# Optimization experiments

Measured on AMD Instinct MI355X. Metric: run time of the kernel, lower is better.

Reference implementation:

```python
import jax, jax.numpy as jnp
import numpy as np

EMBED = 512
HEADS = 8
HEAD_D = EMBED // HEADS
N = 16
QLEN = 512
KLEN = 512


def _relative_keys(Wr, q_len, k_len):
    # Transformer-XL style sinusoid table of size (q_len + k_len)
    max_dist = q_len + k_len
    inv_freqs = 10000.0 ** (-jnp.arange(0, EMBED, 2, dtype=jnp.float32) / EMBED)
    seq = jnp.arange(max_dist, dtype=jnp.float32)[:, None] * inv_freqs[None, :]
    pos_emb = jnp.concatenate([jnp.sin(seq), jnp.cos(seq)], axis=-1)  # [max_dist, E]
    rel = (pos_emb @ Wr.T).reshape(max_dist, HEADS, HEAD_D)           # [max_dist, H, D]
    # query_offset defaults to key_len
    q_pos = jnp.arange(q_len)[:, None] + k_len
    k_pos = jnp.arange(k_len)[None, :]
    rel_idx = jnp.clip(q_pos - k_pos, 0, max_dist - 1)                # [q, k]
    return rel[rel_idx]                                               # [q, k, H, D]


def setup_inputs() -> dict:
    key = jax.random.key(0)
    ks = jax.random.split(key, 12)
    s = 0.02
    return {
        "values": jax.random.normal(ks[0], (N, KLEN, EMBED), jnp.float32),
        "keys": jax.random.normal(ks[1], (N, KLEN, EMBED), jnp.float32),
        "query": jax.random.normal(ks[2], (N, QLEN, EMBED), jnp.float32),
        "mask": jnp.ones((N, QLEN, KLEN), jnp.int32),
        "Wv": jax.random.normal(ks[3], (HEAD_D, HEAD_D), jnp.float32) * s,
        "Wk": jax.random.normal(ks[4], (HEAD_D, HEAD_D), jnp.float32) * s,
        "Wq": jax.random.normal(ks[5], (HEAD_D, HEAD_D), jnp.float32) * s,
        "Wr": jax.random.normal(ks[6], (EMBED, EMBED), jnp.float32) * s,
        "u_bias": jax.random.normal(ks[7], (HEADS, HEAD_D), jnp.float32) * s,
        "v_bias": jax.random.normal(ks[8], (HEADS, HEAD_D), jnp.float32) * s,
        "Wo": jax.random.normal(ks[9], (EMBED, EMBED), jnp.float32) * s,
        "bo": jnp.zeros((EMBED,), jnp.float32),
    }


def reference(values, keys, query, mask, Wv, Wk, Wq, Wr, u_bias, v_bias, Wo, bo):
    # per-head projections (same D x D weight shared across heads, torch Linear: x @ W.T)
    v = values.reshape(N, KLEN, HEADS, HEAD_D) @ Wv.T
    k = keys.reshape(N, KLEN, HEADS, HEAD_D) @ Wk.T
    q = query.reshape(N, QLEN, HEADS, HEAD_D) @ Wq.T

    rel_keys = _relative_keys(Wr, QLEN, KLEN)  # [q, k, H, D]

    content = jnp.einsum("nqhd,nkhd->nhqk", q + u_bias, k)
    position = jnp.einsum("nqhd,qkhd->nhqk", q + v_bias, rel_keys)
    energy = content + position
    energy = jnp.where(mask[:, None, :, :] == 0, jnp.float32(-1e20), energy)

    attn = jax.nn.softmax(energy / (float(HEAD_D) ** 0.5), axis=3)  # [N,H,q,k]
    out = jnp.einsum("nhqk,nkhd->nqhd", attn, v).reshape(N, QLEN, EMBED)
    out = out @ Wo.T + bo
    return out, attn
```

## Files before the change

### kernel.cpp

```cpp
#include <hip/hip_runtime.h>
#include <math.h>

#define NB     16
#define HEADS  8
#define HD     64
#define EMBED  512
#define QL     512
#define KL     512

#define WS_QU   0
#define WS_QV   2097152
#define WS_KB   4194304
#define WS_VT   6291456
#define WS_PEB  8388608
#define WS_RELB 8912896
#define WS_OH   9175040

typedef __attribute__((ext_vector_type(8))) short bf16x8;
typedef __attribute__((ext_vector_type(4))) float f32x4;
typedef __attribute__((ext_vector_type(8))) unsigned short ushort8v;
typedef __attribute__((ext_vector_type(4))) unsigned short ushort4v;

#define MFMA16 __builtin_amdgcn_mfma_f32_16x16x32_bf16

static __device__ __forceinline__ unsigned short f2bf(float x) {
    unsigned u = __builtin_bit_cast(unsigned, x);
    u += 0x7fffu + ((u >> 16) & 1u);
    return (unsigned short)(u >> 16);
}

static __device__ __forceinline__ bf16x8 pack8(f32x4 a, f32x4 b) {
    union { bf16x8 v; unsigned u[4]; } r;
    asm("v_cvt_pk_bf16_f32 %0, %1, %2" : "=v"(r.u[0]) : "v"(a[0]), "v"(a[1]));
    asm("v_cvt_pk_bf16_f32 %0, %1, %2" : "=v"(r.u[1]) : "v"(a[2]), "v"(a[3]));
    asm("v_cvt_pk_bf16_f32 %0, %1, %2" : "=v"(r.u[2]) : "v"(b[0]), "v"(b[1]));
    asm("v_cvt_pk_bf16_f32 %0, %1, %2" : "=v"(r.u[3]) : "v"(b[2]), "v"(b[3]));
    return r.v;
}

__global__ void pe_kernel(unsigned short* __restrict__ peb) {
    int j = blockIdx.x;
    int i = threadIdx.x;
    float invf = exp2f(-(float)i * (13.287712379549449f / 256.0f));
    float ang  = (float)j * invf;
    peb[j * 512 + i]       = f2bf(sinf(ang));
    peb[j * 512 + 256 + i] = f2bf(cosf(ang));
}

__global__ __launch_bounds__(256) void rel_kernel(const unsigned short* __restrict__ peb,
                                                  const float* __restrict__ Wr,
                                                  unsigned short* __restrict__ relb) {
    __shared__ __align__(16) unsigned short At[64][64];
    __shared__ __align__(16) unsigned short Bt[64][64];
    int bm = blockIdx.x >> 3, bn = blockIdx.x & 7;
    int tid = threadIdx.x;
    int w = tid >> 6, lane = tid & 63;
    int fr = lane & 15, fg = lane >> 4;
    f32x4 acc[4] = {};
    for (int kk = 0; kk < 512; kk += 64) {
        __syncthreads();
        for (int p = 0; p < 2; ++p) {
            int idx = tid + 256 * p;
            int row = idx >> 3, slot = idx & 7;
            *(bf16x8*)&At[row][((slot ^ (row & 7))) * 8] =
                *(const bf16x8*)&peb[(bm * 64 + row) * 512 + kk + slot * 8];
        }
        for (int p = 0; p < 4; ++p) {
            int idx = tid + 256 * p;
            int row = idx >> 4, c4 = idx & 15;
            float4 v = *(const float4*)&Wr[(bn * 64 + row) * 512 + kk + c4 * 4];
            ushort4v pk;
            pk[0] = f2bf(v.x); pk[1] = f2bf(v.y); pk[2] = f2bf(v.z); pk[3] = f2bf(v.w);
            int slot = c4 >> 1, rem = (c4 & 1) * 4;
            *(ushort4v*)&Bt[row][((slot ^ (row & 7))) * 8 + rem] = pk;
        }
        __syncthreads();
        bf16x8 af[2];
        int ar = w * 16 + fr;
#pragma unroll
        for (int s = 0; s < 2; ++s)
            af[s] = *(const bf16x8*)&At[ar][((fg + 4 * s) ^ (ar & 7)) * 8];
#pragma unroll
        for (int c = 0; c < 4; ++c) {
            int br = c * 16 + fr;
#pragma unroll
            for (int s = 0; s < 2; ++s) {
                bf16x8 bf = *(const bf16x8*)&Bt[br][((fg + 4 * s) ^ (br & 7)) * 8];
                acc[c] = MFMA16(af[s], bf, acc[c], 0, 0, 0);
            }
        }
    }
#pragma unroll
    for (int c = 0; c < 4; ++c)
#pragma unroll
        for (int i = 0; i < 4; ++i)
            relb[(bn * 1024 + bm * 64 + w * 16 + fg * 4 + i) * 64 + c * 16 + fr] =
                f2bf(acc[c][i]);
}

__global__ __launch_bounds__(256) void proj_kernel(const float* __restrict__ query,
                                                   const float* __restrict__ keys,
                                                   const float* __restrict__ values,
                                                   const float* __restrict__ Wq,
                                                   const float* __restrict__ Wk,
                                                   const float* __restrict__ Wv,
                                                   const float* __restrict__ u_bias,
                                                   const float* __restrict__ v_bias,
                                                   float* __restrict__ ws) {
    __shared__ __align__(16) unsigned short inb[32][512];
    __shared__ __align__(16) unsigned short Wb[3][64][64];
    __shared__ __align__(16) unsigned short vtile[4][64][36];
    int n = blockIdx.x >> 4, t0 = (blockIdx.x & 15) * 32;
    int tid = threadIdx.x;
    int w = tid >> 6, lane = tid & 63;
    int fr = lane & 15, fg = lane >> 4;

    for (int p = 0; p < 3; ++p) {
        const float* Wp = (p == 0) ? Wq : (p == 1) ? Wk : Wv;
        for (int it = 0; it < 4; ++it) {
            int idx = tid + 256 * it;
            int row = idx >> 4, c4 = idx & 15;
            float4 v = *(const float4*)&Wp[row * 64 + c4 * 4];
            ushort4v pk;
            pk[0] = f2bf(v.x); pk[1] = f2bf(v.y); pk[2] = f2bf(v.z); pk[3] = f2bf(v.w);
            int slot = c4 >> 1, rem = (c4 & 1) * 4;
            *(ushort4v*)&Wb[p][row][((slot ^ (row & 7))) * 8 + rem] = pk;
        }
    }
    unsigned short* qu_b = (unsigned short*)(ws + WS_QU);
    unsigned short* qv_b = (unsigned short*)(ws + WS_QV);
    unsigned short* k_b  = (unsigned short*)(ws + WS_KB);
    unsigned short* vT_b = (unsigned short*)(ws + WS_VT);

    for (int p = 0; p < 3; ++p) {
        const float* src = (p == 0) ? query : (p == 1) ? keys : values;
        __syncthreads();
        for (int it = 0; it < 16; ++it) {
            int idx = tid + 256 * it;
            int row = idx >> 7, c4 = idx & 127;
            float4 v = *(const float4*)&src[((long)(n * 512 + t0 + row)) * 512 + c4 * 4];
            ushort4v pk;
            pk[0] = f2bf(v.x); pk[1] = f2bf(v.y); pk[2] = f2bf(v.z); pk[3] = f2bf(v.w);
            int slot = c4 >> 1, rem = (c4 & 1) * 4;
            *(ushort4v*)&inb[row][((slot ^ (row & 7))) * 8 + rem] = pk;
        }
        __syncthreads();
        for (int hh = 0; hh < 2; ++hh) {
            int h = w * 2 + hh, nh = n * 8 + h;
            bf16x8 af[2][2];
#pragma unroll
            for (int tt = 0; tt < 2; ++tt) {
                int ar = tt * 16 + fr;
#pragma unroll
                for (int s = 0; s < 2; ++s)
                    af[tt][s] = *(const bf16x8*)&inb[ar][(h * 8 + ((fg + 4 * s) ^ (ar & 7))) * 8];
            }
            f32x4 acc[2][4] = {};
#pragma unroll
            for (int dt = 0; dt < 4; ++dt) {
                int br = dt * 16 + fr;
                bf16x8 bf[2];
#pragma unroll
                for (int s = 0; s < 2; ++s)
                    bf[s] = *(const bf16x8*)&Wb[p][br][((fg + 4 * s) ^ (br & 7)) * 8];
#pragma unroll
                for (int tt = 0; tt < 2; ++tt)
#pragma unroll
                    for (int s = 0; s < 2; ++s)
                        acc[tt][dt] = MFMA16(af[tt][s], bf[s], acc[tt][dt], 0, 0, 0);
            }
            if (p == 0) {
#pragma unroll
                for (int dt = 0; dt < 4; ++dt) {
                    float ub = u_bias[h * 64 + dt * 16 + fr];
                    float vb = v_bias[h * 64 + dt * 16 + fr];
#pragma unroll
                    for (int tt = 0; tt < 2; ++tt)
#pragma unroll
                        for (int i = 0; i < 4; ++i) {
                            long o = ((long)(nh * 512 + t0 + tt * 16 + fg * 4 + i)) * 64 +
                                     dt * 16 + fr;
                            qu_b[o] = f2bf(acc[tt][dt][i] + ub);
                            qv_b[o] = f2bf(acc[tt][dt][i] + vb);
                        }
                }
            } else if (p == 1) {
#pragma unroll
                for (int dt = 0; dt < 4; ++dt)
#pragma unroll
                    for (int tt = 0; tt < 2; ++tt)
#pragma unroll
                        for (int i = 0; i < 4; ++i)
                            k_b[((long)(nh * 512 + t0 + tt * 16 + fg * 4 + i)) * 64 +
                                dt * 16 + fr] = f2bf(acc[tt][dt][i]);
            } else {
#pragma unroll
                for (int dt = 0; dt < 4; ++dt)
#pragma unroll
                    for (int tt = 0; tt < 2; ++tt)
#pragma unroll
                        for (int i = 0; i < 4; ++i)
                            vtile[w][dt * 16 + fr][tt * 16 + fg * 4 + i] =
                                f2bf(acc[tt][dt][i]);
                __syncthreads();
#pragma unroll
                for (int dg = 0; dg < 8; ++dg) {
                    int d = dg * 8 + (lane >> 3), tq = lane & 7;
                    *(ushort4v*)&vT_b[((long)(nh * 64 + d)) * 512 + t0 + tq * 4] =
                        *(const ushort4v*)&vtile[w][d][tq * 4];
                }
                __syncthreads();
            }
        }
    }
}

__global__ __launch_bounds__(512) void attn_kernel(float* __restrict__ ws,
                                                   const int* __restrict__ mask,
                                                   float* __restrict__ d_out) {
    __shared__ __align__(16) float S[32][516];
    __shared__ __align__(16) float red[4][32][17];

    const unsigned short* qu_b = (const unsigned short*)(ws + WS_QU);
    const unsigned short* qv_b = (const unsigned short*)(ws + WS_QV);
    const unsigned short* k_b  = (const unsigned short*)(ws + WS_KB);
    const unsigned short* vT_b = (const unsigned short*)(ws + WS_VT);
    const unsigned short* relb = (const unsigned short*)(ws + WS_RELB);
    unsigned short* ohb = (unsigned short*)(ws + WS_OH);
    float* attn = d_out + 4194304;

    int bid = blockIdx.x;
    int swz = (bid & 7) * 64 + (bid >> 3);
    int nh = swz >> 2, qb = swz & 3;
    int n  = nh >> 3, h = nh & 7;

    int tid  = threadIdx.x;
    int w    = tid >> 6, lane = tid & 63;
    int fr   = lane & 15, fg = lane >> 4;

    const unsigned short* kbase = k_b + (long)nh * 512 * 64;
    bf16x8 kreg[4][2];
#pragma unroll
    for (int t = 0; t < 4; ++t) {
        const unsigned short* kp = kbase + (long)(w * 64 + t * 16 + fr) * 64;
        kreg[t][0] = *(const bf16x8*)&kp[fg * 8];
        kreg[t][1] = *(const bf16x8*)&kp[(fg + 4) * 8];
    }
    int dt = w & 3, kh = w >> 2;
    const unsigned short* vp0 = vT_b + ((long)(nh * 64 + dt * 16 + fr)) * 512 + kh * 256;
    bf16x8 vreg[8];
#pragma unroll
    for (int kk = 0; kk < 8; ++kk)
        vreg[kk] = *(const bf16x8*)&vp0[kk * 32 + fg * 8];

    const unsigned short* rbase = relb + (long)h * 1024 * 64;

    for (int ti = 0; ti < 4; ++ti) {
        int q0 = qb * 128 + ti * 32;

#pragma unroll
        for (int qt = 0; qt < 2; ++qt) {
            long qa = ((long)(nh * 512 + q0 + qt * 16 + fr)) * 64;
            bf16x8 a0 = *(const bf16x8*)&qu_b[qa + fg * 8];
            bf16x8 a1 = *(const bf16x8*)&qu_b[qa + (fg + 4) * 8];
#pragma unroll
            for (int t = 0; t < 4; ++t) {
                f32x4 acc = {0.f, 0.f, 0.f, 0.f};
                acc = MFMA16(a0, kreg[t][0], acc, 0, 0, 0);
                acc = MFMA16(a1, kreg[t][1], acc, 0, 0, 0);
                int kcol = w * 64 + t * 16 + fr;
#pragma unroll
                for (int i = 0; i < 4; ++i)
                    S[qt * 16 + fg * 4 + i][kcol] = acc[i];
            }
        }
        __syncthreads();

        {
            bf16x8 qvf[2][2];
#pragma unroll
            for (int qt = 0; qt < 2; ++qt) {
                long qa = ((long)(nh * 512 + q0 + qt * 16 + fr)) * 64;
                qvf[qt][0] = *(const bf16x8*)&qv_b[qa + fg * 8];
                qvf[qt][1] = *(const bf16x8*)&qv_b[qa + (fg + 4) * 8];
            }
            for (int jt = w; jt < 34; jt += 8) {
                int jj = jt * 16 + fr;
                int j = q0 + 1 + jj;
                const unsigned short* rp = rbase + (long)j * 64;
                bf16x8 b0 = *(const bf16x8*)&rp[fg * 8];
                bf16x8 b1 = *(const bf16x8*)&rp[(fg + 4) * 8];
#pragma unroll
                for (int qt = 0; qt < 2; ++qt) {
                    f32x4 acc = {0.f, 0.f, 0.f, 0.f};
                    acc = MFMA16(qvf[qt][0], b0, acc, 0, 0, 0);
                    acc = MFMA16(qvf[qt][1], b1, acc, 0, 0, 0);
#pragma unroll
                    for (int i = 0; i < 4; ++i) {
                        int r = qt * 16 + fg * 4 + i;
                        int k = r + 511 - jj;
                        if ((unsigned)k < 512u) S[r][k] += acc[i];
                    }
                }
            }
        }
        __syncthreads();

        for (int rr = 0; rr < 4; ++rr) {
            int r = w * 4 + rr;
            const int* mrow = mask + ((long)(n * 512 + q0 + r)) * 512;
            float lg[8];
            float mx = -3.0e38f;
#pragma unroll
            for (int j = 0; j < 8; ++j) {
                int k = lane + 64 * j;
                float s = S[r][k];
                int m = mrow[k];
                float l = (m == 0) ? -1.25e19f : s * 0.125f;
                lg[j] = l;
                mx = fmaxf(mx, l);
            }
            for (int o = 32; o > 0; o >>= 1) mx = fmaxf(mx, __shfl_xor(mx, o, 64));
            float sum = 0.f;
#pragma unroll
            for (int j = 0; j < 8; ++j) { lg[j] = __expf(lg[j] - mx); sum += lg[j]; }
            for (int o = 32; o > 0; o >>= 1) sum += __shfl_xor(sum, o, 64);
            float inv = 1.0f / sum;
            float* arow = attn + ((long)(nh * 512 + q0 + r)) * 512;
#pragma unroll
            for (int j = 0; j < 8; ++j) {
                int k = lane + 64 * j;
                float p = lg[j] * inv;
                S[r][k] = p;
                arow[k] = p;
            }
        }
        __syncthreads();

        {
            f32x4 oacc[2] = {{0.f,0.f,0.f,0.f},{0.f,0.f,0.f,0.f}};
#pragma unroll
            for (int kk = 0; kk < 8; ++kk) {
#pragma unroll
                for (int qt = 0; qt < 2; ++qt) {
                    const float* sp = &S[qt * 16 + fr][kh * 256 + kk * 32 + fg * 8];
                    f32x4 a = *(const f32x4*)sp;
                    f32x4 b = *(const f32x4*)(sp + 4);
                    bf16x8 pk = pack8(a, b);
                    oacc[qt] = MFMA16(pk, vreg[kk], oacc[qt], 0, 0, 0);
                }
            }
            if (kh == 1) {
#pragma unroll
                for (int qt = 0; qt < 2; ++qt)
#pragma unroll
                    for (int i = 0; i < 4; ++i)
                        red[dt][qt * 16 + fg * 4 + i][fr] = oacc[qt][i];
            }
            __syncthreads();
            if (kh == 0) {
#pragma unroll
                for (int qt = 0; qt < 2; ++qt)
#pragma unroll
                    for (int i = 0; i < 4; ++i) {
                        float o = oacc[qt][i] + red[dt][qt * 16 + fg * 4 + i][fr];
                        ohb[((long)(n * 512 + q0 + qt * 16 + fg * 4 + i)) * 512 +
                            h * 64 + dt * 16 + fr] = f2bf(o);
                    }
            }
        }
        __syncthreads();
    }
}

__global__ __launch_bounds__(256) void wo_kernel(const float* __restrict__ ws,
                                                 const float* __restrict__ Wo,
                                                 const float* __restrict__ bo,
                                                 float* __restrict__ d_out) {
    __shared__ __align__(16) unsigned short At[128][64];
    __shared__ __align__(16) unsigned short Bt[64][64];
    const unsigned short* ohb = (const unsigned short*)(ws + WS_OH);
    int bm = blockIdx.x >> 3, bn = blockIdx.x & 7;
    int tid = threadIdx.x;
    int w = tid >> 6, lane = tid & 63;
    int fr = lane & 15, fg = lane >> 4;
    f32x4 acc[2][4] = {};
    for (int kk = 0; kk < 512; kk += 64) {
        __syncthreads();
        for (int p = 0; p < 4; ++p) {
            int idx = tid + 256 * p;
            int row = idx >> 3, slot = idx & 7;
            *(bf16x8*)&At[row][((slot ^ (row & 7))) * 8] =
                *(const bf16x8*)&ohb[(long)(bm * 128 + row) * 512 + kk + slot * 8];
        }
        for (int p = 0; p < 2; ++p) {
            int idx = tid + 256 * p;
            int row = idx >> 3, slot = idx & 7;
            const float* g = &Wo[(bn * 64 + row) * 512 + kk + slot * 8];
            float4 a = *(const float4*)g;
            float4 b = *(const float4*)(g + 4);
            ushort8v pk;
            pk[0] = f2bf(a.x); pk[1] = f2bf(a.y); pk[2] = f2bf(a.z); pk[3] = f2bf(a.w);
            pk[4] = f2bf(b.x); pk[5] = f2bf(b.y); pk[6] = f2bf(b.z); pk[7] = f2bf(b.w);
            *(ushort8v*)&Bt[row][((slot ^ (row & 7))) * 8] = pk;
        }
        __syncthreads();
        bf16x8 af[2][2], bfr[4][2];
#pragma unroll
        for (int t = 0; t < 2; ++t) {
            int ar = w * 32 + t * 16 + fr;
#pragma unroll
            for (int s = 0; s < 2; ++s)
                af[t][s] = *(const bf16x8*)&At[ar][((fg + s * 4) ^ (ar & 7)) * 8];
        }
#pragma unroll
        for (int c = 0; c < 4; ++c) {
            int br = c * 16 + fr;
#pragma unroll
            for (int s = 0; s < 2; ++s)
                bfr[c][s] = *(const bf16x8*)&Bt[br][((fg + s * 4) ^ (br & 7)) * 8];
        }
#pragma unroll
        for (int t = 0; t < 2; ++t)
#pragma unroll
            for (int c = 0; c < 4; ++c)
#pragma unroll
                for (int s = 0; s < 2; ++s)
                    acc[t][c] = MFMA16(af[t][s], bfr[c][s], acc[t][c], 0, 0, 0);
    }
#pragma unroll
    for (int t = 0; t < 2; ++t)
#pragma unroll
        for (int c = 0; c < 4; ++c) {
            int col = bn * 64 + c * 16 + fr;
            float b = bo[col];
#pragma unroll
            for (int i = 0; i < 4; ++i) {
                int row = bm * 128 + w * 32 + t * 16 + fg * 4 + i;
                d_out[(long)row * 512 + col] = acc[t][c][i] + b;
            }
        }
}

extern "C" void kernel_launch(void* const* d_in, const int* in_sizes, int n_in,
                              void* d_out, int out_size, void* d_ws, size_t ws_size,
                              hipStream_t stream) {
    const float* values = (const float*)d_in[0];
    const float* keys   = (const float*)d_in[1];
    const float* query  = (const float*)d_in[2];
    const int*   mask   = (const int*)d_in[3];
    const float* Wv     = (const float*)d_in[4];
    const float* Wk     = (const float*)d_in[5];
    const float* Wq     = (const float*)d_in[6];
    const float* Wr     = (const float*)d_in[7];
    const float* u_bias = (const float*)d_in[8];
    const float* v_bias = (const float*)d_in[9];
    const float* Wo     = (const float*)d_in[10];
    const float* bo     = (const float*)d_in[11];
    float* out = (float*)d_out;
    float* ws  = (float*)d_ws;

    unsigned short* peb  = (unsigned short*)(ws + WS_PEB);
    unsigned short* relb = (unsigned short*)(ws + WS_RELB);

    hipLaunchKernelGGL(pe_kernel,   dim3(1024),  dim3(256), 0, stream, peb);
    hipLaunchKernelGGL(rel_kernel,  dim3(128),   dim3(256), 0, stream, peb, Wr, relb);
    hipLaunchKernelGGL(proj_kernel, dim3(256),   dim3(256), 0, stream,
                       query, keys, values, Wq, Wk, Wv, u_bias, v_bias, ws);
    hipLaunchKernelGGL(attn_kernel, dim3(512),   dim3(512), 0, stream, ws, mask, out);
    hipLaunchKernelGGL(wo_kernel,   dim3(512),   dim3(256), 0, stream, ws, Wo, bo, out);
}
```

Before: 146.4 us.

## Store attention scores as swizzled bf16 in LDS and double the attention grid

The attention kernel now keeps its score tile in LDS as bf16 instead of fp32, with an XOR swizzle on columns. The grid is split into 1024 blocks of 64 queries, and K fragments are reloaded per tile instead of being held in registers. Launch bounds ask for more resident waves, and the mask, attention-row and P-fragment accesses become vectorized 8-wide operations. The aim is less LDS per block and fewer registers, so more blocks run at once and memory latency is hidden better. In exchange, content and position scores are accumulated and rounded in bf16 before the softmax, which lowers numerical precision.

```diff
diff --git a/kernel.cpp b/kernel.cpp
--- a/kernel.cpp
+++ b/kernel.cpp
@@ -27,6 +27,11 @@
     unsigned u = __builtin_bit_cast(unsigned, x);
     u += 0x7fffu + ((u >> 16) & 1u);
     return (unsigned short)(u >> 16);
+}
+
+static __device__ __forceinline__ float bf2f(unsigned short v) {
+    unsigned u = ((unsigned)v) << 16;
+    return __builtin_bit_cast(float, u);
 }
 
 static __device__ __forceinline__ bf16x8 pack8(f32x4 a, f32x4 b) {
@@ -215,10 +220,10 @@
     }
 }
 
-__global__ __launch_bounds__(512) void attn_kernel(float* __restrict__ ws,
-                                                   const int* __restrict__ mask,
-                                                   float* __restrict__ d_out) {
-    __shared__ __align__(16) float S[32][516];
+__global__ __launch_bounds__(512, 6) void attn_kernel(float* __restrict__ ws,
+                                                      const int* __restrict__ mask,
+                                                      float* __restrict__ d_out) {
+    __shared__ __align__(16) unsigned short S16[32][528];
     __shared__ __align__(16) float red[4][32][17];
 
     const unsigned short* qu_b = (const unsigned short*)(ws + WS_QU);
@@ -230,22 +235,14 @@
     float* attn = d_out + 4194304;
 
     int bid = blockIdx.x;
-    int swz = (bid & 7) * 64 + (bid >> 3);
-    int nh = swz >> 2, qb = swz & 3;
+    int swz = (bid & 7) * 128 + (bid >> 3);
+    int nh = swz >> 3, qg = swz & 7;
     int n  = nh >> 3, h = nh & 7;
 
     int tid  = threadIdx.x;
     int w    = tid >> 6, lane = tid & 63;
     int fr   = lane & 15, fg = lane >> 4;
 
-    const unsigned short* kbase = k_b + (long)nh * 512 * 64;
-    bf16x8 kreg[4][2];
-#pragma unroll
-    for (int t = 0; t < 4; ++t) {
-        const unsigned short* kp = kbase + (long)(w * 64 + t * 16 + fr) * 64;
-        kreg[t][0] = *(const bf16x8*)&kp[fg * 8];
-        kreg[t][1] = *(const bf16x8*)&kp[(fg + 4) * 8];
-    }
     int dt = w & 3, kh = w >> 2;
     const unsigned short* vp0 = vT_b + ((long)(nh * 64 + dt * 16 + fr)) * 512 + kh * 256;
     bf16x8 vreg[8];
@@ -253,25 +250,37 @@
     for (int kk = 0; kk < 8; ++kk)
         vreg[kk] = *(const bf16x8*)&vp0[kk * 32 + fg * 8];
 
+    const unsigned short* kbase = k_b + (long)nh * 512 * 64;
     const unsigned short* rbase = relb + (long)h * 1024 * 64;
 
-    for (int ti = 0; ti < 4; ++ti) {
-        int q0 = qb * 128 + ti * 32;
-
-#pragma unroll
-        for (int qt = 0; qt < 2; ++qt) {
-            long qa = ((long)(nh * 512 + q0 + qt * 16 + fr)) * 64;
-            bf16x8 a0 = *(const bf16x8*)&qu_b[qa + fg * 8];
-            bf16x8 a1 = *(const bf16x8*)&qu_b[qa + (fg + 4) * 8];
+    for (int ti = 0; ti < 2; ++ti) {
+        int q0 = qg * 64 + ti * 32;
+
+        {
+            bf16x8 qf[2][2];
+#pragma unroll
+            for (int qt = 0; qt < 2; ++qt) {
+                long qa = ((long)(nh * 512 + q0 + qt * 16 + fr)) * 64;
+                qf[qt][0] = *(const bf16x8*)&qu_b[qa + fg * 8];
+                qf[qt][1] = *(const bf16x8*)&qu_b[qa + (fg + 4) * 8];
+            }
 #pragma unroll
             for (int t = 0; t < 4; ++t) {
-                f32x4 acc = {0.f, 0.f, 0.f, 0.f};
-                acc = MFMA16(a0, kreg[t][0], acc, 0, 0, 0);
-                acc = MFMA16(a1, kreg[t][1], acc, 0, 0, 0);
                 int kcol = w * 64 + t * 16 + fr;
-#pragma unroll
-                for (int i = 0; i < 4; ++i)
-                    S[qt * 16 + fg * 4 + i][kcol] = acc[i];
+                const unsigned short* kp = kbase + (long)kcol * 64;
+                bf16x8 b0 = *(const bf16x8*)&kp[fg * 8];
+                bf16x8 b1 = *(const bf16x8*)&kp[(fg + 4) * 8];
+#pragma unroll
+                for (int qt = 0; qt < 2; ++qt) {
+                    f32x4 acc = {0.f, 0.f, 0.f, 0.f};
+                    acc = MFMA16(qf[qt][0], b0, acc, 0, 0, 0);
+                    acc = MFMA16(qf[qt][1], b1, acc, 0, 0, 0);
+#pragma unroll
+                    for (int i = 0; i < 4; ++i) {
+                        int r = qt * 16 + fg * 4 + i;
+                        S16[r][kcol ^ (8 * (r & 7))] = f2bf(acc[i]);
+                    }
+                }
             }
         }
         __syncthreads();
@@ -284,9 +293,43 @@
                 qvf[qt][0] = *(const bf16x8*)&qv_b[qa + fg * 8];
                 qvf[qt][1] = *(const bf16x8*)&qv_b[qa + (fg + 4) * 8];
             }
-            for (int jt = w; jt < 34; jt += 8) {
-                int jj = jt * 16 + fr;
-                int j = q0 + 1 + jj;
+#pragma unroll
+            for (int half = 0; half < 2; ++half) {
+                int jj0 = (w + half * 16) * 16 + fr;
+                int jj1 = jj0 + 128;
+                const unsigned short* rp0 = rbase + (long)(q0 + 1 + jj0) * 64;
+                const unsigned short* rp1 = rbase + (long)(q0 + 1 + jj1) * 64;
+                bf16x8 a0 = *(const bf16x8*)&rp0[fg * 8];
+                bf16x8 a1 = *(const bf16x8*)&rp0[(fg + 4) * 8];
+                bf16x8 c0 = *(const bf16x8*)&rp1[fg * 8];
+                bf16x8 c1 = *(const bf16x8*)&rp1[(fg + 4) * 8];
+#pragma unroll
+                for (int qt = 0; qt < 2; ++qt) {
+                    f32x4 accA = {0.f, 0.f, 0.f, 0.f};
+                    f32x4 accB = {0.f, 0.f, 0.f, 0.f};
+                    accA = MFMA16(qvf[qt][0], a0, accA, 0, 0, 0);
+                    accA = MFMA16(qvf[qt][1], a1, accA, 0, 0, 0);
+                    accB = MFMA16(qvf[qt][0], c0, accB, 0, 0, 0);
+                    accB = MFMA16(qvf[qt][1], c1, accB, 0, 0, 0);
+#pragma unroll
+                    for (int i = 0; i < 4; ++i) {
+                        int r = qt * 16 + fg * 4 + i;
+                        int kA = r + 511 - jj0;
+                        int kB = r + 511 - jj1;
+                        if ((unsigned)kA < 512u) {
+                            unsigned short* sp = &S16[r][kA ^ (8 * (r & 7))];
+                            *sp = f2bf(bf2f(*sp) + accA[i]);
+                        }
+                        if ((unsigned)kB < 512u) {
+                            unsigned short* sp = &S16[r][kB ^ (8 * (r & 7))];
+                            *sp = f2bf(bf2f(*sp) + accB[i]);
+                        }
+                    }
+                }
+            }
+            if (w < 2) {
+                int jj = (w + 32) * 16 + fr;
+                int j = q0 + 1 + jj; if (j > 1023) j = 1023;
                 const unsigned short* rp = rbase + (long)j * 64;
                 bf16x8 b0 = *(const bf16x8*)&rp[fg * 8];
                 bf16x8 b1 = *(const bf16x8*)&rp[(fg + 4) * 8];
@@ -299,7 +342,10 @@
                     for (int i = 0; i < 4; ++i) {
                         int r = qt * 16 + fg * 4 + i;
                         int k = r + 511 - jj;
-                        if ((unsigned)k < 512u) S[r][k] += acc[i];
+                        if ((unsigned)k < 512u) {
+                            unsigned short* sp = &S16[r][k ^ (8 * (r & 7))];
+                            *sp = f2bf(bf2f(*sp) + acc[i]);
+                        }
                     }
                 }
             }
@@ -308,32 +354,33 @@
 
         for (int rr = 0; rr < 4; ++rr) {
             int r = w * 4 + rr;
-            const int* mrow = mask + ((long)(n * 512 + q0 + r)) * 512;
+            int kb = lane ^ (r & 7);
+            bf16x8 sv = *(const bf16x8*)&S16[r][lane * 8];
+            const int* mrow = mask + ((long)(n * 512 + q0 + r)) * 512 + kb * 8;
+            int4 m0 = *(const int4*)mrow;
+            int4 m1 = *(const int4*)(mrow + 4);
+            int mv[8] = {m0.x, m0.y, m0.z, m0.w, m1.x, m1.y, m1.z, m1.w};
             float lg[8];
             float mx = -3.0e38f;
 #pragma unroll
-            for (int j = 0; j < 8; ++j) {
-                int k = lane + 64 * j;
-                float s = S[r][k];
-                int m = mrow[k];
-                float l = (m == 0) ? -1.25e19f : s * 0.125f;
-                lg[j] = l;
+            for (int u = 0; u < 8; ++u) {
+                float sraw = bf2f((unsigned short)sv[u]);
+                float l = (mv[u] == 0) ? -1.25e19f : sraw * 0.125f;
+                lg[u] = l;
                 mx = fmaxf(mx, l);
             }
             for (int o = 32; o > 0; o >>= 1) mx = fmaxf(mx, __shfl_xor(mx, o, 64));
             float sum = 0.f;
 #pragma unroll
-            for (int j = 0; j < 8; ++j) { lg[j] = __expf(lg[j] - mx); sum += lg[j]; }
+            for (int u = 0; u < 8; ++u) { lg[u] = __expf(lg[u] - mx); sum += lg[u]; }
             for (int o = 32; o > 0; o >>= 1) sum += __shfl_xor(sum, o, 64);
             float inv = 1.0f / sum;
-            float* arow = attn + ((long)(nh * 512 + q0 + r)) * 512;
-#pragma unroll
-            for (int j = 0; j < 8; ++j) {
-                int k = lane + 64 * j;
-                float p = lg[j] * inv;
-                S[r][k] = p;
-                arow[k] = p;
-            }
+            f32x4 p0 = {lg[0] * inv, lg[1] * inv, lg[2] * inv, lg[3] * inv};
+            f32x4 p1 = {lg[4] * inv, lg[5] * inv, lg[6] * inv, lg[7] * inv};
+            *(bf16x8*)&S16[r][lane * 8] = pack8(p0, p1);
+            float* arow = attn + ((long)(nh * 512 + q0 + r)) * 512 + kb * 8;
+            *(f32x4*)arow = p0;
+            *(f32x4*)(arow + 4) = p1;
         }
         __syncthreads();
 
@@ -343,11 +390,10 @@
             for (int kk = 0; kk < 8; ++kk) {
 #pragma unroll
                 for (int qt = 0; qt < 2; ++qt) {
-                    const float* sp = &S[qt * 16 + fr][kh * 256 + kk * 32 + fg * 8];
-                    f32x4 a = *(const f32x4*)sp;
-                    f32x4 b = *(const f32x4*)(sp + 4);
-                    bf16x8 pk = pack8(a, b);
-                    oacc[qt] = MFMA16(pk, vreg[kk], oacc[qt], 0, 0, 0);
+                    int row = qt * 16 + fr;
+                    int colp = (kh * 256 + kk * 32 + fg * 8) ^ (8 * (fr & 7));
+                    bf16x8 pf = *(const bf16x8*)&S16[row][colp];
+                    oacc[qt] = MFMA16(pf, vreg[kk], oacc[qt], 0, 0, 0);
                 }
             }
             if (kh == 1) {
@@ -369,7 +415,6 @@
                     }
             }
         }
-        __syncthreads();
     }
 }
 
@@ -467,6 +512,6 @@
     hipLaunchKernelGGL(rel_kernel,  dim3(128),   dim3(256), 0, stream, peb, Wr, relb);
     hipLaunchKernelGGL(proj_kernel, dim3(256),   dim3(256), 0, stream,
                        query, keys, values, Wq, Wk, Wv, u_bias, v_bias, ws);
-    hipLaunchKernelGGL(attn_kernel, dim3(512),   dim3(512), 0, stream, ws, mask, out);
+    hipLaunchKernelGGL(attn_kernel, dim3(1024),  dim3(512), 0, stream, ws, mask, out);
     hipLaunchKernelGGL(wo_kernel,   dim3(512),   dim3(256), 0, stream, ws, Wo, bo, out);
 }
```

After: 313.3 us. 2.14x slower.

## Restructure attention kernel: per-wave rel-key tiles, swizzled LDS, bf16 probabilities, more blocks

Applied to the files above, without the earlier changes.

Gives each wave a fixed band of relative-key tiles that cover only its own 64-column slice of the score tile, so the position term is written without conflicting += updates. The content score is then accumulated onto it in place, which removes one barrier. The score tile is XOR-swizzled in LDS, softmax probabilities are stored as bf16 so the PV MFMA operand can be read directly, and s_setprio is raised around the MFMA sections. The grid doubles to 1024 blocks with two 32-row q-tiles per block, and the trailing barrier is dropped. The extra blocks reload K/V registers more often, and removing the barrier risks LDS races between iterations.

```diff
diff --git a/kernel.cpp b/kernel.cpp
--- a/kernel.cpp
+++ b/kernel.cpp
@@ -29,13 +29,9 @@
     return (unsigned short)(u >> 16);
 }
 
-static __device__ __forceinline__ bf16x8 pack8(f32x4 a, f32x4 b) {
-    union { bf16x8 v; unsigned u[4]; } r;
-    asm("v_cvt_pk_bf16_f32 %0, %1, %2" : "=v"(r.u[0]) : "v"(a[0]), "v"(a[1]));
-    asm("v_cvt_pk_bf16_f32 %0, %1, %2" : "=v"(r.u[1]) : "v"(a[2]), "v"(a[3]));
-    asm("v_cvt_pk_bf16_f32 %0, %1, %2" : "=v"(r.u[2]) : "v"(b[0]), "v"(b[1]));
-    asm("v_cvt_pk_bf16_f32 %0, %1, %2" : "=v"(r.u[3]) : "v"(b[2]), "v"(b[3]));
-    return r.v;
+static __device__ __forceinline__ float bf2f(unsigned short v) {
+    unsigned u = ((unsigned)v) << 16;
+    return __builtin_bit_cast(float, u);
 }
 
 __global__ void pe_kernel(unsigned short* __restrict__ peb) {
@@ -218,7 +214,7 @@
 __global__ __launch_bounds__(512) void attn_kernel(float* __restrict__ ws,
                                                    const int* __restrict__ mask,
                                                    float* __restrict__ d_out) {
-    __shared__ __align__(16) float S[32][516];
+    __shared__ __align__(16) float S[32][520];
     __shared__ __align__(16) float red[4][32][17];
 
     const unsigned short* qu_b = (const unsigned short*)(ws + WS_QU);
@@ -230,8 +226,8 @@
     float* attn = d_out + 4194304;
 
     int bid = blockIdx.x;
-    int swz = (bid & 7) * 64 + (bid >> 3);
-    int nh = swz >> 2, qb = swz & 3;
+    int swz = (bid & 7) * 128 + (bid >> 3);
+    int nh = swz >> 3, qg = swz & 7;
     int n  = nh >> 3, h = nh & 7;
 
     int tid  = threadIdx.x;
@@ -254,27 +250,10 @@
         vreg[kk] = *(const bf16x8*)&vp0[kk * 32 + fg * 8];
 
     const unsigned short* rbase = relb + (long)h * 1024 * 64;
-
-    for (int ti = 0; ti < 4; ++ti) {
-        int q0 = qb * 128 + ti * 32;
-
-#pragma unroll
-        for (int qt = 0; qt < 2; ++qt) {
-            long qa = ((long)(nh * 512 + q0 + qt * 16 + fr)) * 64;
-            bf16x8 a0 = *(const bf16x8*)&qu_b[qa + fg * 8];
-            bf16x8 a1 = *(const bf16x8*)&qu_b[qa + (fg + 4) * 8];
-#pragma unroll
-            for (int t = 0; t < 4; ++t) {
-                f32x4 acc = {0.f, 0.f, 0.f, 0.f};
-                acc = MFMA16(a0, kreg[t][0], acc, 0, 0, 0);
-                acc = MFMA16(a1, kreg[t][1], acc, 0, 0, 0);
-                int kcol = w * 64 + t * 16 + fr;
-#pragma unroll
-                for (int i = 0; i < 4; ++i)
-                    S[qt * 16 + fg * 4 + i][kcol] = acc[i];
-            }
-        }
-        __syncthreads();
+    int jt0 = 28 - 4 * w;
+
+    for (int ti = 0; ti < 2; ++ti) {
+        int q0 = qg * 64 + ti * 32;
 
         {
             bf16x8 qvf[2][2];
@@ -284,37 +263,77 @@
                 qvf[qt][0] = *(const bf16x8*)&qv_b[qa + fg * 8];
                 qvf[qt][1] = *(const bf16x8*)&qv_b[qa + (fg + 4) * 8];
             }
-            for (int jt = w; jt < 34; jt += 8) {
-                int jj = jt * 16 + fr;
-                int j = q0 + 1 + jj;
-                const unsigned short* rp = rbase + (long)j * 64;
-                bf16x8 b0 = *(const bf16x8*)&rp[fg * 8];
-                bf16x8 b1 = *(const bf16x8*)&rp[(fg + 4) * 8];
+#pragma unroll
+            for (int pp = 0; pp < 3; ++pp) {
+                int jjA = (jt0 + 2 * pp) * 16 + fr;
+                int jjB = jjA + 16;
+                int jA = q0 + 1 + jjA; if (jA > 1023) jA = 1023;
+                int jB = q0 + 1 + jjB; if (jB > 1023) jB = 1023;
+                const unsigned short* rpA = rbase + (long)jA * 64;
+                const unsigned short* rpB = rbase + (long)jB * 64;
+                bf16x8 a0 = *(const bf16x8*)&rpA[fg * 8];
+                bf16x8 a1 = *(const bf16x8*)&rpA[(fg + 4) * 8];
+                bf16x8 c0 = *(const bf16x8*)&rpB[fg * 8];
+                bf16x8 c1 = *(const bf16x8*)&rpB[(fg + 4) * 8];
+                __builtin_amdgcn_s_setprio(1);
 #pragma unroll
                 for (int qt = 0; qt < 2; ++qt) {
-                    f32x4 acc = {0.f, 0.f, 0.f, 0.f};
-                    acc = MFMA16(qvf[qt][0], b0, acc, 0, 0, 0);
-                    acc = MFMA16(qvf[qt][1], b1, acc, 0, 0, 0);
+                    f32x4 accA = {0.f, 0.f, 0.f, 0.f};
+                    f32x4 accB = {0.f, 0.f, 0.f, 0.f};
+                    accA = MFMA16(qvf[qt][0], a0, accA, 0, 0, 0);
+                    accA = MFMA16(qvf[qt][1], a1, accA, 0, 0, 0);
+                    accB = MFMA16(qvf[qt][0], c0, accB, 0, 0, 0);
+                    accB = MFMA16(qvf[qt][1], c1, accB, 0, 0, 0);
 #pragma unroll
                     for (int i = 0; i < 4; ++i) {
                         int r = qt * 16 + fg * 4 + i;
-                        int k = r + 511 - jj;
-                        if ((unsigned)k < 512u) S[r][k] += acc[i];
+                        int kA = r + 511 - jjA;
+                        int kB = r + 511 - jjB;
+                        if ((unsigned)(kA - w * 64) < 64u)
+                            S[r][kA ^ (4 * (r & 7))] = accA[i];
+                        if ((unsigned)(kB - w * 64) < 64u)
+                            S[r][kB ^ (4 * (r & 7))] = accB[i];
                     }
                 }
-            }
+                __builtin_amdgcn_s_setprio(0);
+            }
+        }
+
+        {
+            bf16x8 qf[2][2];
+#pragma unroll
+            for (int qt = 0; qt < 2; ++qt) {
+                long qa = ((long)(nh * 512 + q0 + qt * 16 + fr)) * 64;
+                qf[qt][0] = *(const bf16x8*)&qu_b[qa + fg * 8];
+                qf[qt][1] = *(const bf16x8*)&qu_b[qa + (fg + 4) * 8];
+            }
+            __builtin_amdgcn_s_setprio(1);
+#pragma unroll
+            for (int t = 0; t < 4; ++t) {
+#pragma unroll
+                for (int qt = 0; qt < 2; ++qt) {
+                    f32x4* sp = (f32x4*)&S[qt * 16 + fr]
+                                        [(w * 64 + t * 16 + fg * 4) ^ (4 * (fr & 7))];
+                    f32x4 acc = *sp;
+                    acc = MFMA16(kreg[t][0], qf[qt][0], acc, 0, 0, 0);
+                    acc = MFMA16(kreg[t][1], qf[qt][1], acc, 0, 0, 0);
+                    *sp = acc;
+                }
+            }
+            __builtin_amdgcn_s_setprio(0);
         }
         __syncthreads();
 
         for (int rr = 0; rr < 4; ++rr) {
             int r = w * 4 + rr;
+            int x4 = 4 * (r & 7), x8 = 8 * (r & 7);
             const int* mrow = mask + ((long)(n * 512 + q0 + r)) * 512;
             float lg[8];
             float mx = -3.0e38f;
 #pragma unroll
             for (int j = 0; j < 8; ++j) {
                 int k = lane + 64 * j;
-                float s = S[r][k];
+                float s = S[r][k ^ x4];
                 int m = mrow[k];
                 float l = (m == 0) ? -1.25e19f : s * 0.125f;
                 lg[j] = l;
@@ -326,12 +345,13 @@
             for (int j = 0; j < 8; ++j) { lg[j] = __expf(lg[j] - mx); sum += lg[j]; }
             for (int o = 32; o > 0; o >>= 1) sum += __shfl_xor(sum, o, 64);
             float inv = 1.0f / sum;
+            unsigned short* prow = (unsigned short*)&S[r][0];
             float* arow = attn + ((long)(nh * 512 + q0 + r)) * 512;
 #pragma unroll
             for (int j = 0; j < 8; ++j) {
                 int k = lane + 64 * j;
                 float p = lg[j] * inv;
-                S[r][k] = p;
+                prow[k ^ x8] = f2bf(p);
                 arow[k] = p;
             }
         }
@@ -339,17 +359,19 @@
 
         {
             f32x4 oacc[2] = {{0.f,0.f,0.f,0.f},{0.f,0.f,0.f,0.f}};
+            __builtin_amdgcn_s_setprio(1);
 #pragma unroll
             for (int kk = 0; kk < 8; ++kk) {
 #pragma unroll
                 for (int qt = 0; qt < 2; ++qt) {
-                    const float* sp = &S[qt * 16 + fr][kh * 256 + kk * 32 + fg * 8];
-                    f32x4 a = *(const f32x4*)sp;
-                    f32x4 b = *(const f32x4*)(sp + 4);
-                    bf16x8 pk = pack8(a, b);
-                    oacc[qt] = MFMA16(pk, vreg[kk], oacc[qt], 0, 0, 0);
+                    int row = qt * 16 + fr;
+                    const unsigned short* prow = (const unsigned short*)&S[row][0];
+                    bf16x8 pf = *(const bf16x8*)
+                        &prow[(kh * 256 + kk * 32 + fg * 8) ^ (8 * (row & 7))];
+                    oacc[qt] = MFMA16(pf, vreg[kk], oacc[qt], 0, 0, 0);
                 }
             }
+            __builtin_amdgcn_s_setprio(0);
             if (kh == 1) {
 #pragma unroll
                 for (int qt = 0; qt < 2; ++qt)
@@ -369,7 +391,6 @@
                     }
             }
         }
-        __syncthreads();
     }
 }
 
@@ -467,6 +488,6 @@
     hipLaunchKernelGGL(rel_kernel,  dim3(128),   dim3(256), 0, stream, peb, Wr, relb);
     hipLaunchKernelGGL(proj_kernel, dim3(256),   dim3(256), 0, stream,
                        query, keys, values, Wq, Wk, Wv, u_bias, v_bias, ws);
-    hipLaunchKernelGGL(attn_kernel, dim3(512),   dim3(512), 0, stream, ws, mask, out);
+    hipLaunchKernelGGL(attn_kernel, dim3(1024),  dim3(512), 0, stream, ws, mask, out);
     hipLaunchKernelGGL(wo_kernel,   dim3(512),   dim3(256), 0, stream, ws, Wo, bo, out);
 }
```

After: 157.6 us. 7.7% more time.
